# Performance work log

Measured on AMD Instinct MI355X. Metric: run time of the kernel, lower is better.

Reference implementation:

```python
import jax, jax.numpy as jnp
import numpy as np

K = 2            # number of kernel experts (1 common + 1 learned)
TEMPERATURE = 31.0
STRIDE = (2, 2)
KSIZE = 5


def setup_inputs() -> dict:
    key = jax.random.key(0)
    ks = jax.random.split(key, 7)
    B, Cin, H, W = 128, 96, 63, 63
    Cout = 256
    x = jax.random.normal(ks[0], (B, Cin, H, W), jnp.float32)
    common_weight = jax.random.normal(ks[1], (1, Cout, Cin, KSIZE, KSIZE), jnp.float32) * 0.05
    common_bias = jax.random.normal(ks[2], (1, Cout), jnp.float32) * 0.01
    expert_weight = jax.random.normal(ks[3], (1, Cout, Cin, KSIZE, KSIZE), jnp.float32) * 0.05
    expert_bias = jax.random.normal(ks[4], (1, Cout), jnp.float32) * 0.01
    att_w1 = jax.random.normal(ks[5], (24, Cin), jnp.float32) * 0.1   # fc1: 1x1 conv == linear
    att_w2 = jax.random.normal(ks[6], (K, 24), jnp.float32) * 0.1     # fc2
    return {"x": x, "common_weight": common_weight, "common_bias": common_bias,
            "expert_weight": expert_weight, "expert_bias": expert_bias,
            "att_w1": att_w1, "att_w2": att_w2}


def reference(x, common_weight, common_bias, expert_weight, expert_bias, att_w1, att_w2):
    B, Cin, H, W = x.shape
    Cout = common_weight.shape[1]

    # attention2d: global average pool -> fc1 -> relu -> fc2 -> softmax(logits / T)
    pooled = jnp.mean(x, axis=(2, 3))                       # [B, Cin]
    hidden = jax.nn.relu(pooled @ att_w1.T)                 # [B, 24]
    logits = hidden @ att_w2.T                              # [B, K]
    att = jax.nn.softmax(logits / TEMPERATURE, axis=1)      # [B, K]

    # aggregate per-sample kernels: [B,K] @ [K, Cout*Cin*k*k]
    weight = jnp.concatenate([common_weight, expert_weight], axis=0).reshape(K, -1)
    agg_w = (att @ weight).reshape(B * Cout, Cin, KSIZE, KSIZE)
    bias2 = jnp.concatenate([common_bias, expert_bias], axis=0)  # [K, Cout]
    agg_b = (att @ bias2).reshape(-1)                            # [B*Cout]

    # grouped conv with groups = batch_size (per-sample conv)
    xg = x.reshape(1, B * Cin, H, W)
    out = jax.lax.conv_general_dilated(
        xg, agg_w, window_strides=STRIDE, padding='VALID',
        feature_group_count=B,
        dimension_numbers=('NCHW', 'OIHW', 'NCHW'))             # [1, B*Cout, Ho, Wo]
    out = out + agg_b[None, :, None, None]
    Ho, Wo = out.shape[2], out.shape[3]
    return out.reshape(B, Cout, Ho, Wo)
```

## Files before the change

### kernel.cpp

```cpp
#include <hip/hip_runtime.h>
#include <math.h>

#define CIN   96
#define HW_IN 3969
#define WIN   63
#define COUT  256
#define NPIX  900
#define WO    30
#define KTOT  2400
#define NB    128
#define KSTEPS 75
#define AGG_OFF 65536
#define AGG_BYTES ((size_t)NB * 2 * KSTEPS * 8192)

typedef short bf16x8 __attribute__((ext_vector_type(8)));
typedef float f32x4  __attribute__((ext_vector_type(4)));
typedef __attribute__((address_space(1))) const void gas_t;
typedef __attribute__((address_space(3))) void las_t;

__device__ __forceinline__ unsigned pk2(float lo, float hi) {
  unsigned r;
  asm("v_cvt_pk_bf16_f32 %0, %1, %2" : "=v"(r) : "v"(lo), "v"(hi));
  return r;
}

__global__ __launch_bounds__(256) void pool_kernel(const float* __restrict__ x,
                                                   float* __restrict__ pooled) {
  const int ci = blockIdx.x;
  const int b  = blockIdx.y;
  const float* xc = x + ((size_t)b * CIN + ci) * HW_IN;
  const int tid = threadIdx.x, lane = tid & 63, wv = tid >> 6;
  float s = 0.f;
  const int head = (4 - (ci & 3)) & 3;
  if (tid < head) s += xc[tid];
  const float4* x4 = (const float4*)(xc + head);
  const int n4 = (HW_IN - head) >> 2;
  for (int i = tid; i < n4; i += 256) { float4 v = x4[i]; s += (v.x + v.y) + (v.z + v.w); }
  const int done = head + (n4 << 2);
  if (tid < HW_IN - done) s += xc[done + tid];
  #pragma unroll
  for (int off = 32; off > 0; off >>= 1) s += __shfl_xor(s, off, 64);
  __shared__ float part[4];
  if (lane == 0) part[wv] = s;
  __syncthreads();
  if (tid == 0)
    pooled[(size_t)b * CIN + ci] = (part[0] + part[1] + part[2] + part[3]) * (1.0f / HW_IN);
}

__global__ __launch_bounds__(64) void attn_kernel(const float* __restrict__ pooled,
                                                  const float* __restrict__ w1,
                                                  const float* __restrict__ w2,
                                                  float* __restrict__ att) {
  const int b = blockIdx.x;
  const int tid = threadIdx.x;
  __shared__ float hidden[24];
  const float* pb = pooled + (size_t)b * CIN;
  if (tid < 24) {
    float h = 0.f;
    const float* w1r = w1 + tid * CIN;
    for (int ci = 0; ci < CIN; ++ci) h += pb[ci] * w1r[ci];
    hidden[tid] = fmaxf(h, 0.f);
  }
  __syncthreads();
  if (tid == 0) {
    float l0 = 0.f, l1 = 0.f;
    for (int j = 0; j < 24; ++j) { l0 += hidden[j] * w2[j]; l1 += hidden[j] * w2[24 + j]; }
    l0 *= (1.0f / 31.0f); l1 *= (1.0f / 31.0f);
    const float m = fmaxf(l0, l1);
    const float e0 = expf(l0 - m), e1 = expf(l1 - m);
    const float inv = 1.0f / (e0 + e1);
    att[b * 2 + 0] = e0 * inv;
    att[b * 2 + 1] = e1 * inv;
  }
}

__global__ __launch_bounds__(256) void agg_kernel(const float* __restrict__ wc,
                                                  const float* __restrict__ we,
                                                  const float* __restrict__ att,
                                                  unsigned* __restrict__ aggW) {
  const int ks = blockIdx.x;
  const int t  = blockIdx.y;
  const int b  = blockIdx.z;
  const float a0 = att[b * 2 + 0];
  const float a1 = att[b * 2 + 1];
  unsigned* dst = aggW + ((size_t)((b * 2 + t) * KSTEPS + ks) << 11);
  #pragma unroll
  for (int uu = 0; uu < 2; ++uu) {
    const int u = threadIdx.x + uu * 256;
    const int row = u >> 2, slot = u & 3;
    const int oct = slot ^ ((row >> 1) & 3);
    const float* pc = wc + (size_t)(t * 128 + row) * KTOT + ks * 32 + oct * 8;
    const float* pe = we + (size_t)(t * 128 + row) * KTOT + ks * 32 + oct * 8;
    float4 c0 = ((const float4*)pc)[0], c1 = ((const float4*)pc)[1];
    float4 e0 = ((const float4*)pe)[0], e1 = ((const float4*)pe)[1];
    uint4 q;
    q.x = pk2(a0 * c0.x + a1 * e0.x, a0 * c0.y + a1 * e0.y);
    q.y = pk2(a0 * c0.z + a1 * e0.z, a0 * c0.w + a1 * e0.w);
    q.z = pk2(a0 * c1.x + a1 * e1.x, a0 * c1.y + a1 * e1.y);
    q.w = pk2(a0 * c1.z + a1 * e1.z, a0 * c1.w + a1 * e1.w);
    ((uint4*)dst)[u] = q;
  }
}

__global__ __launch_bounds__(256) void conv_pre(
    const float* __restrict__ x,
    const float* __restrict__ bc, const float* __restrict__ be,
    const float* __restrict__ att, const unsigned* __restrict__ aggW,
    float* __restrict__ out) {
  const int flat = (int)(blockIdx.x + (blockIdx.y << 3) + (blockIdx.z << 4));
  const int wg   = ((flat & 7) << 8) | (flat >> 3);
  const int p0 = (wg & 7) * 128;
  const int m0 = ((wg >> 3) & 1) * 128;
  const int b  = wg >> 4;

  __shared__ short As[2][128 * 32];
  __shared__ short Bs[2][128][40];
  __shared__ int   koffAll[KTOT];
  __shared__ float biasS[128];

  const int tid  = threadIdx.x;
  const int wv   = tid >> 6, lane = tid & 63;
  const int quad = lane >> 4, lm = lane & 15;
  const int wm = (wv >> 1) * 64;
  const int wn = (wv & 1) * 64;

  if (tid < 128) {
    const float a0 = att[b * 2 + 0], a1 = att[b * 2 + 1];
    biasS[tid] = a0 * bc[m0 + tid] + a1 * be[m0 + tid];
  }
  for (int k = tid; k < KTOT; k += 256) {
    const int ci = k / 25, r = k - ci * 25;
    const int kh = r / 5,  kw = r - kh * 5;
    koffAll[k] = ci * HW_IN + kh * WIN + kw;
  }

  const int rowT = tid >> 2;
  const int oct  = (tid & 3) * 8;

  const float* xb = x + (size_t)b * (CIN * HW_IN);
  const int pA = p0 + rowT, pB = p0 + rowT + 64;
  const int ohA = pA / WO, owA = pA - ohA * WO;
  const int ohB = pB / WO, owB = pB - ohB * WO;
  const bool vA = pA < NPIX, vB = pB < NPIX;
  const float* xpA = xb + (ohA * 2) * WIN + owA * 2;
  const float* xpB = xb + (ohB * 2) * WIN + owB * 2;

  const char* aggB = (const char*)aggW
                   + ((size_t)((b * 2 + (m0 >> 7)) * KSTEPS) << 13)
                   + (((wv << 7) + lane) << 4);
  const int xoct = quad ^ ((lm >> 1) & 3);

  const f32x4 zero = {0.f, 0.f, 0.f, 0.f};
  f32x4 acc[4][4];
  #pragma unroll
  for (int i = 0; i < 4; ++i)
    #pragma unroll
    for (int j = 0; j < 4; ++j) acc[i][j] = zero;

  __syncthreads();

  {
    __builtin_amdgcn_global_load_lds((gas_t*)aggB, (las_t*)&As[0][wv << 10], 16, 0, 0);
    __builtin_amdgcn_global_load_lds((gas_t*)(aggB + 1024), (las_t*)&As[0][(wv << 10) + 512], 16, 0, 0);
    const int4 ka = *(const int4*)&koffAll[oct];
    const int4 kb = *(const int4*)&koffAll[oct + 4];
    uint4 qa = {0u, 0u, 0u, 0u}, qb = {0u, 0u, 0u, 0u};
    if (vA) {
      qa.x = pk2(xpA[ka.x], xpA[ka.y]); qa.y = pk2(xpA[ka.z], xpA[ka.w]);
      qa.z = pk2(xpA[kb.x], xpA[kb.y]); qa.w = pk2(xpA[kb.z], xpA[kb.w]);
    }
    if (vB) {
      qb.x = pk2(xpB[ka.x], xpB[ka.y]); qb.y = pk2(xpB[ka.z], xpB[ka.w]);
      qb.z = pk2(xpB[kb.x], xpB[kb.y]); qb.w = pk2(xpB[kb.z], xpB[kb.w]);
    }
    *(uint4*)&Bs[0][rowT][oct] = qa;
    *(uint4*)&Bs[0][rowT + 64][oct] = qb;
  }
  __syncthreads();

  int cur = 0;
  for (int ks = 0; ks < KSTEPS - 1; ++ks) {
    const int nxt = cur ^ 1;
    const char* src = aggB + ((size_t)(ks + 1) << 13);
    __builtin_amdgcn_global_load_lds((gas_t*)src, (las_t*)&As[nxt][wv << 10], 16, 0, 0);
    __builtin_amdgcn_global_load_lds((gas_t*)(src + 1024), (las_t*)&As[nxt][(wv << 10) + 512], 16, 0, 0);
    const int k0n = (ks + 1) * 32;
    const int4 ka = *(const int4*)&koffAll[k0n + oct];
    const int4 kb = *(const int4*)&koffAll[k0n + oct + 4];
    float g0 = 0.f, g1 = 0.f, g2 = 0.f, g3 = 0.f, g4 = 0.f, g5 = 0.f, g6 = 0.f, g7 = 0.f;
    float h0 = 0.f, h1 = 0.f, h2 = 0.f, h3 = 0.f, h4 = 0.f, h5 = 0.f, h6 = 0.f, h7 = 0.f;
    if (vA) {
      g0 = xpA[ka.x]; g1 = xpA[ka.y]; g2 = xpA[ka.z]; g3 = xpA[ka.w];
      g4 = xpA[kb.x]; g5 = xpA[kb.y]; g6 = xpA[kb.z]; g7 = xpA[kb.w];
    }
    if (vB) {
      h0 = xpB[ka.x]; h1 = xpB[ka.y]; h2 = xpB[ka.z]; h3 = xpB[ka.w];
      h4 = xpB[kb.x]; h5 = xpB[kb.y]; h6 = xpB[kb.z]; h7 = xpB[kb.w];
    }
    bf16x8 af[4], bfv[4];
    #pragma unroll
    for (int i = 0; i < 4; ++i)
      af[i] = *(const bf16x8*)&As[cur][(wm + i * 16 + lm) * 32 + xoct * 8];
    #pragma unroll
    for (int j = 0; j < 4; ++j)
      bfv[j] = *(const bf16x8*)&Bs[cur][wn + j * 16 + lm][quad * 8];
    #pragma unroll
    for (int i = 0; i < 4; ++i)
      #pragma unroll
      for (int j = 0; j < 4; ++j)
        acc[i][j] = __builtin_amdgcn_mfma_f32_16x16x32_bf16(af[i], bfv[j], acc[i][j], 0, 0, 0);
    uint4 qa, qb;
    qa.x = pk2(g0, g1); qa.y = pk2(g2, g3); qa.z = pk2(g4, g5); qa.w = pk2(g6, g7);
    qb.x = pk2(h0, h1); qb.y = pk2(h2, h3); qb.z = pk2(h4, h5); qb.w = pk2(h6, h7);
    *(uint4*)&Bs[nxt][rowT][oct] = qa;
    *(uint4*)&Bs[nxt][rowT + 64][oct] = qb;
    __syncthreads();
    cur = nxt;
  }

  {
    bf16x8 af[4], bfv[4];
    #pragma unroll
    for (int i = 0; i < 4; ++i)
      af[i] = *(const bf16x8*)&As[cur][(wm + i * 16 + lm) * 32 + xoct * 8];
    #pragma unroll
    for (int j = 0; j < 4; ++j)
      bfv[j] = *(const bf16x8*)&Bs[cur][wn + j * 16 + lm][quad * 8];
    #pragma unroll
    for (int i = 0; i < 4; ++i)
      #pragma unroll
      for (int j = 0; j < 4; ++j)
        acc[i][j] = __builtin_amdgcn_mfma_f32_16x16x32_bf16(af[i], bfv[j], acc[i][j], 0, 0, 0);
  }

  float* outb = out + ((size_t)b * COUT + m0) * NPIX;
  #pragma unroll
  for (int j = 0; j < 4; ++j) {
    const int p = p0 + wn + j * 16 + lm;
    if (p < NPIX) {
      #pragma unroll
      for (int i = 0; i < 4; ++i) {
        #pragma unroll
        for (int r = 0; r < 4; ++r) {
          const int m = wm + i * 16 + quad * 4 + r;
          outb[(size_t)m * NPIX + p] = acc[i][j][r] + biasS[m];
        }
      }
    }
  }
}

__global__ __launch_bounds__(256) void conv_fb(
    const float* __restrict__ x,
    const float* __restrict__ wc, const float* __restrict__ we,
    const float* __restrict__ bc, const float* __restrict__ be,
    const float* __restrict__ att, float* __restrict__ out) {
  const int flat = (int)(blockIdx.x + (blockIdx.y << 3) + (blockIdx.z << 4));
  const int wg   = ((flat & 7) << 8) | (flat >> 3);
  const int p0 = (wg & 7) * 128;
  const int m0 = ((wg >> 3) & 1) * 128;
  const int b  = wg >> 4;

  __shared__ short As[128 * 40];
  __shared__ short Bs[128][40];
  __shared__ int   koffAll[KTOT];
  __shared__ float biasS[128];

  const int tid  = threadIdx.x;
  const int wv   = tid >> 6, lane = tid & 63;
  const int quad = lane >> 4, lm = lane & 15;
  const int wm = (wv >> 1) * 64;
  const int wn = (wv & 1) * 64;

  const float a0 = att[b * 2 + 0];
  const float a1 = att[b * 2 + 1];

  if (tid < 128) biasS[tid] = a0 * bc[m0 + tid] + a1 * be[m0 + tid];
  for (int k = tid; k < KTOT; k += 256) {
    const int ci = k / 25, r = k - ci * 25;
    const int kh = r / 5,  kw = r - kh * 5;
    koffAll[k] = ci * HW_IN + kh * WIN + kw;
  }

  const int rowT = tid >> 2;
  const int oct  = (tid & 3) * 8;

  const float* xb = x + (size_t)b * (CIN * HW_IN);
  const int pA = p0 + rowT, pB = p0 + rowT + 64;
  const int ohA = pA / WO, owA = pA - ohA * WO;
  const int ohB = pB / WO, owB = pB - ohB * WO;
  const bool vA = pA < NPIX, vB = pB < NPIX;
  const float* xpA = xb + (ohA * 2) * WIN + owA * 2;
  const float* xpB = xb + (ohB * 2) * WIN + owB * 2;

  const float* wcr0 = wc + (size_t)(m0 + rowT) * KTOT + oct;
  const float* wer0 = we + (size_t)(m0 + rowT) * KTOT + oct;

  const f32x4 zero = {0.f, 0.f, 0.f, 0.f};
  f32x4 acc[4][4];
  #pragma unroll
  for (int i = 0; i < 4; ++i)
    #pragma unroll
    for (int j = 0; j < 4; ++j) acc[i][j] = zero;

  for (int k0 = 0; k0 < KTOT; k0 += 32) {
    __syncthreads();
    #pragma unroll
    for (int t = 0; t < 2; ++t) {
      const float4* pc = (const float4*)(wcr0 + (size_t)t * 64 * KTOT + k0);
      const float4* pe = (const float4*)(wer0 + (size_t)t * 64 * KTOT + k0);
      float4 c0 = pc[0], c1 = pc[1];
      float4 e0 = pe[0], e1 = pe[1];
      uint4 q;
      q.x = pk2(a0 * c0.x + a1 * e0.x, a0 * c0.y + a1 * e0.y);
      q.y = pk2(a0 * c0.z + a1 * e0.z, a0 * c0.w + a1 * e0.w);
      q.z = pk2(a0 * c1.x + a1 * e1.x, a0 * c1.y + a1 * e1.y);
      q.w = pk2(a0 * c1.z + a1 * e1.z, a0 * c1.w + a1 * e1.w);
      *(uint4*)&As[(rowT + t * 64) * 40 + oct] = q;
    }
    const int4 ka = *(const int4*)&koffAll[k0 + oct];
    const int4 kb = *(const int4*)&koffAll[k0 + oct + 4];
    {
      uint4 q = {0u, 0u, 0u, 0u};
      if (vA) {
        q.x = pk2(xpA[ka.x], xpA[ka.y]); q.y = pk2(xpA[ka.z], xpA[ka.w]);
        q.z = pk2(xpA[kb.x], xpA[kb.y]); q.w = pk2(xpA[kb.z], xpA[kb.w]);
      }
      *(uint4*)&Bs[rowT][oct] = q;
    }
    {
      uint4 q = {0u, 0u, 0u, 0u};
      if (vB) {
        q.x = pk2(xpB[ka.x], xpB[ka.y]); q.y = pk2(xpB[ka.z], xpB[ka.w]);
        q.z = pk2(xpB[kb.x], xpB[kb.y]); q.w = pk2(xpB[kb.z], xpB[kb.w]);
      }
      *(uint4*)&Bs[rowT + 64][oct] = q;
    }
    __syncthreads();
    bf16x8 af[4], bfv[4];
    #pragma unroll
    for (int i = 0; i < 4; ++i) af[i]  = *(const bf16x8*)&As[(wm + i * 16 + lm) * 40 + quad * 8];
    #pragma unroll
    for (int j = 0; j < 4; ++j) bfv[j] = *(const bf16x8*)&Bs[wn + j * 16 + lm][quad * 8];
    #pragma unroll
    for (int i = 0; i < 4; ++i)
      #pragma unroll
      for (int j = 0; j < 4; ++j)
        acc[i][j] = __builtin_amdgcn_mfma_f32_16x16x32_bf16(af[i], bfv[j], acc[i][j], 0, 0, 0);
  }

  float* outb = out + ((size_t)b * COUT + m0) * NPIX;
  #pragma unroll
  for (int j = 0; j < 4; ++j) {
    const int p = p0 + wn + j * 16 + lm;
    if (p < NPIX) {
      #pragma unroll
      for (int i = 0; i < 4; ++i) {
        #pragma unroll
        for (int r = 0; r < 4; ++r) {
          const int m = wm + i * 16 + quad * 4 + r;
          outb[(size_t)m * NPIX + p] = acc[i][j][r] + biasS[m];
        }
      }
    }
  }
}

extern "C" void kernel_launch(void* const* d_in, const int* in_sizes, int n_in,
                              void* d_out, int out_size, void* d_ws, size_t ws_size,
                              hipStream_t stream) {
  (void)in_sizes; (void)n_in; (void)out_size;
  const float* x  = (const float*)d_in[0];
  const float* wc = (const float*)d_in[1];
  const float* bc = (const float*)d_in[2];
  const float* we = (const float*)d_in[3];
  const float* be = (const float*)d_in[4];
  const float* w1 = (const float*)d_in[5];
  const float* w2 = (const float*)d_in[6];
  float* out = (float*)d_out;

  float* att    = (float*)d_ws;
  float* pooled = att + 256;
  unsigned* aggW = (unsigned*)((char*)d_ws + AGG_OFF);

  pool_kernel<<<dim3(CIN, NB), 256, 0, stream>>>(x, pooled);
  attn_kernel<<<NB, 64, 0, stream>>>(pooled, w1, w2, att);

  if (ws_size >= AGG_OFF + AGG_BYTES) {
    agg_kernel<<<dim3(KSTEPS, 2, NB), 256, 0, stream>>>(wc, we, att, aggW);
    conv_pre<<<dim3(8, 2, NB), 256, 0, stream>>>(x, bc, be, att, aggW, out);
  } else {
    conv_fb<<<dim3(8, 2, NB), 256, 0, stream>>>(x, wc, we, bc, be, att, out);
  }
}
```

Before: 745.9 us.

## Deepen conv GEMM pipeline with triple-buffered A and register-prefetched im2col gathers

Restructures the main loop into a deeper software pipeline. Weight tiles are triple-buffered in LDS and prefetched two steps ahead, and the im2col gathers of x are issued two steps ahead into alternating register arrays. Partial waits (vmcnt) plus raw s_barrier replace __syncthreads, MFMA priority is raised with setprio, and the B tile uses an XOR-swizzled unpadded layout. Out-of-range pixels are clamped rather than predicated, which removes branches at the cost of redundant loads, and the extra register arrays raise register pressure.

```diff
diff --git a/kernel.cpp b/kernel.cpp
--- a/kernel.cpp
+++ b/kernel.cpp
@@ -113,8 +113,8 @@
   const int m0 = ((wg >> 3) & 1) * 128;
   const int b  = wg >> 4;
 
-  __shared__ short As[2][128 * 32];
-  __shared__ short Bs[2][128][40];
+  __shared__ short As[3][4096];
+  __shared__ short Bs[2][4096];
   __shared__ int   koffAll[KTOT];
   __shared__ float biasS[128];
 
@@ -136,12 +136,14 @@
 
   const int rowT = tid >> 2;
   const int oct  = (tid & 3) * 8;
+  const int bu   = (tid & 3) ^ ((rowT >> 1) & 3);
 
   const float* xb = x + (size_t)b * (CIN * HW_IN);
   const int pA = p0 + rowT, pB = p0 + rowT + 64;
-  const int ohA = pA / WO, owA = pA - ohA * WO;
-  const int ohB = pB / WO, owB = pB - ohB * WO;
-  const bool vA = pA < NPIX, vB = pB < NPIX;
+  const int pAc = pA < NPIX ? pA : NPIX - 1;
+  const int pBc = pB < NPIX ? pB : NPIX - 1;
+  const int ohA = pAc / WO, owA = pAc - ohA * WO;
+  const int ohB = pBc / WO, owB = pBc - ohB * WO;
   const float* xpA = xb + (ohA * 2) * WIN + owA * 2;
   const float* xpB = xb + (ohB * 2) * WIN + owB * 2;
 
@@ -157,75 +159,95 @@
     #pragma unroll
     for (int j = 0; j < 4; ++j) acc[i][j] = zero;
 
+  float gA[16], gB[16];
+
   __syncthreads();
 
   {
+    const int4 ka = *(const int4*)&koffAll[oct];
+    const int4 kb = *(const int4*)&koffAll[oct + 4];
+    gB[0] = xpA[ka.x]; gB[1] = xpA[ka.y]; gB[2] = xpA[ka.z]; gB[3] = xpA[ka.w];
+    gB[4] = xpA[kb.x]; gB[5] = xpA[kb.y]; gB[6] = xpA[kb.z]; gB[7] = xpA[kb.w];
+    gB[8] = xpB[ka.x]; gB[9] = xpB[ka.y]; gB[10] = xpB[ka.z]; gB[11] = xpB[ka.w];
+    gB[12] = xpB[kb.x]; gB[13] = xpB[kb.y]; gB[14] = xpB[kb.z]; gB[15] = xpB[kb.w];
     __builtin_amdgcn_global_load_lds((gas_t*)aggB, (las_t*)&As[0][wv << 10], 16, 0, 0);
     __builtin_amdgcn_global_load_lds((gas_t*)(aggB + 1024), (las_t*)&As[0][(wv << 10) + 512], 16, 0, 0);
-    const int4 ka = *(const int4*)&koffAll[oct];
-    const int4 kb = *(const int4*)&koffAll[oct + 4];
-    uint4 qa = {0u, 0u, 0u, 0u}, qb = {0u, 0u, 0u, 0u};
-    if (vA) {
-      qa.x = pk2(xpA[ka.x], xpA[ka.y]); qa.y = pk2(xpA[ka.z], xpA[ka.w]);
-      qa.z = pk2(xpA[kb.x], xpA[kb.y]); qa.w = pk2(xpA[kb.z], xpA[kb.w]);
-    }
-    if (vB) {
-      qb.x = pk2(xpB[ka.x], xpB[ka.y]); qb.y = pk2(xpB[ka.z], xpB[ka.w]);
-      qb.z = pk2(xpB[kb.x], xpB[kb.y]); qb.w = pk2(xpB[kb.z], xpB[kb.w]);
-    }
-    *(uint4*)&Bs[0][rowT][oct] = qa;
-    *(uint4*)&Bs[0][rowT + 64][oct] = qb;
+    __builtin_amdgcn_global_load_lds((gas_t*)(aggB + 8192), (las_t*)&As[1][wv << 10], 16, 0, 0);
+    __builtin_amdgcn_global_load_lds((gas_t*)(aggB + 8192 + 1024), (las_t*)&As[1][(wv << 10) + 512], 16, 0, 0);
+    const int4 ka1 = *(const int4*)&koffAll[32 + oct];
+    const int4 kb1 = *(const int4*)&koffAll[32 + oct + 4];
+    gA[0] = xpA[ka1.x]; gA[1] = xpA[ka1.y]; gA[2] = xpA[ka1.z]; gA[3] = xpA[ka1.w];
+    gA[4] = xpA[kb1.x]; gA[5] = xpA[kb1.y]; gA[6] = xpA[kb1.z]; gA[7] = xpA[kb1.w];
+    gA[8] = xpB[ka1.x]; gA[9] = xpB[ka1.y]; gA[10] = xpB[ka1.z]; gA[11] = xpB[ka1.w];
+    gA[12] = xpB[kb1.x]; gA[13] = xpB[kb1.y]; gA[14] = xpB[kb1.z]; gA[15] = xpB[kb1.w];
+    uint4 qa, qb;
+    qa.x = pk2(gB[0], gB[1]);  qa.y = pk2(gB[2], gB[3]);
+    qa.z = pk2(gB[4], gB[5]);  qa.w = pk2(gB[6], gB[7]);
+    qb.x = pk2(gB[8], gB[9]);  qb.y = pk2(gB[10], gB[11]);
+    qb.z = pk2(gB[12], gB[13]); qb.w = pk2(gB[14], gB[15]);
+    *(uint4*)&Bs[0][rowT * 32 + bu * 8] = qa;
+    *(uint4*)&Bs[0][(rowT + 64) * 32 + bu * 8] = qb;
   }
   __syncthreads();
 
-  int cur = 0;
-  for (int ks = 0; ks < KSTEPS - 1; ++ks) {
-    const int nxt = cur ^ 1;
-    const char* src = aggB + ((size_t)(ks + 1) << 13);
-    __builtin_amdgcn_global_load_lds((gas_t*)src, (las_t*)&As[nxt][wv << 10], 16, 0, 0);
-    __builtin_amdgcn_global_load_lds((gas_t*)(src + 1024), (las_t*)&As[nxt][(wv << 10) + 512], 16, 0, 0);
-    const int k0n = (ks + 1) * 32;
-    const int4 ka = *(const int4*)&koffAll[k0n + oct];
-    const int4 kb = *(const int4*)&koffAll[k0n + oct + 4];
-    float g0 = 0.f, g1 = 0.f, g2 = 0.f, g3 = 0.f, g4 = 0.f, g5 = 0.f, g6 = 0.f, g7 = 0.f;
-    float h0 = 0.f, h1 = 0.f, h2 = 0.f, h3 = 0.f, h4 = 0.f, h5 = 0.f, h6 = 0.f, h7 = 0.f;
-    if (vA) {
-      g0 = xpA[ka.x]; g1 = xpA[ka.y]; g2 = xpA[ka.z]; g3 = xpA[ka.w];
-      g4 = xpA[kb.x]; g5 = xpA[kb.y]; g6 = xpA[kb.z]; g7 = xpA[kb.w];
-    }
-    if (vB) {
-      h0 = xpB[ka.x]; h1 = xpB[ka.y]; h2 = xpB[ka.z]; h3 = xpB[ka.w];
-      h4 = xpB[kb.x]; h5 = xpB[kb.y]; h6 = xpB[kb.z]; h7 = xpB[kb.w];
-    }
-    bf16x8 af[4], bfv[4];
-    #pragma unroll
-    for (int i = 0; i < 4; ++i)
-      af[i] = *(const bf16x8*)&As[cur][(wm + i * 16 + lm) * 32 + xoct * 8];
-    #pragma unroll
-    for (int j = 0; j < 4; ++j)
-      bfv[j] = *(const bf16x8*)&Bs[cur][wn + j * 16 + lm][quad * 8];
-    #pragma unroll
-    for (int i = 0; i < 4; ++i)
-      #pragma unroll
-      for (int j = 0; j < 4; ++j)
-        acc[i][j] = __builtin_amdgcn_mfma_f32_16x16x32_bf16(af[i], bfv[j], acc[i][j], 0, 0, 0);
-    uint4 qa, qb;
-    qa.x = pk2(g0, g1); qa.y = pk2(g2, g3); qa.z = pk2(g4, g5); qa.w = pk2(g6, g7);
-    qb.x = pk2(h0, h1); qb.y = pk2(h2, h3); qb.z = pk2(h4, h5); qb.w = pk2(h6, h7);
-    *(uint4*)&Bs[nxt][rowT][oct] = qa;
-    *(uint4*)&Bs[nxt][rowT + 64][oct] = qb;
-    __syncthreads();
-    cur = nxt;
-  }
+  int acur = 0, aw = 2;
+
+  #define CONV_STEP(T, GH, GN, BR, BW)                                            \
+  {                                                                               \
+    const int ksn = ((T) + 2 <= 74) ? (T) + 2 : 74;                               \
+    const int4 ka = *(const int4*)&koffAll[ksn * 32 + oct];                       \
+    const int4 kb = *(const int4*)&koffAll[ksn * 32 + oct + 4];                   \
+    GN[0] = xpA[ka.x]; GN[1] = xpA[ka.y]; GN[2] = xpA[ka.z]; GN[3] = xpA[ka.w];   \
+    GN[4] = xpA[kb.x]; GN[5] = xpA[kb.y]; GN[6] = xpA[kb.z]; GN[7] = xpA[kb.w];   \
+    GN[8] = xpB[ka.x]; GN[9] = xpB[ka.y]; GN[10] = xpB[ka.z]; GN[11] = xpB[ka.w]; \
+    GN[12] = xpB[kb.x]; GN[13] = xpB[kb.y]; GN[14] = xpB[kb.z]; GN[15] = xpB[kb.w]; \
+    const char* srcA = aggB + ((size_t)ksn << 13);                                \
+    __builtin_amdgcn_global_load_lds((gas_t*)srcA, (las_t*)&As[aw][wv << 10], 16, 0, 0); \
+    __builtin_amdgcn_global_load_lds((gas_t*)(srcA + 1024), (las_t*)&As[aw][(wv << 10) + 512], 16, 0, 0); \
+    bf16x8 af[4], bfv[4];                                                         \
+    _Pragma("unroll")                                                             \
+    for (int i = 0; i < 4; ++i)                                                   \
+      af[i] = *(const bf16x8*)&As[acur][(wm + i * 16 + lm) * 32 + xoct * 8];      \
+    _Pragma("unroll")                                                             \
+    for (int j = 0; j < 4; ++j)                                                   \
+      bfv[j] = *(const bf16x8*)&Bs[BR][(wn + j * 16 + lm) * 32 + xoct * 8];       \
+    __builtin_amdgcn_s_setprio(1);                                                \
+    _Pragma("unroll")                                                             \
+    for (int i = 0; i < 4; ++i)                                                   \
+      _Pragma("unroll")                                                           \
+      for (int j = 0; j < 4; ++j)                                                 \
+        acc[i][j] = __builtin_amdgcn_mfma_f32_16x16x32_bf16(af[i], bfv[j], acc[i][j], 0, 0, 0); \
+    __builtin_amdgcn_s_setprio(0);                                                \
+    uint4 qa2, qb2;                                                               \
+    qa2.x = pk2(GH[0], GH[1]);  qa2.y = pk2(GH[2], GH[3]);                        \
+    qa2.z = pk2(GH[4], GH[5]);  qa2.w = pk2(GH[6], GH[7]);                        \
+    qb2.x = pk2(GH[8], GH[9]);  qb2.y = pk2(GH[10], GH[11]);                      \
+    qb2.z = pk2(GH[12], GH[13]); qb2.w = pk2(GH[14], GH[15]);                     \
+    *(uint4*)&Bs[BW][rowT * 32 + bu * 8] = qa2;                                   \
+    *(uint4*)&Bs[BW][(rowT + 64) * 32 + bu * 8] = qb2;                            \
+    __builtin_amdgcn_sched_barrier(0);                                            \
+    asm volatile("s_waitcnt vmcnt(18) lgkmcnt(0)" ::: "memory");                  \
+    __builtin_amdgcn_sched_barrier(0);                                            \
+    __builtin_amdgcn_s_barrier();                                                 \
+    __builtin_amdgcn_sched_barrier(0);                                            \
+    acur = (acur == 2) ? 0 : acur + 1;                                            \
+    aw   = (aw == 2) ? 0 : aw + 1;                                                \
+  }
+
+  for (int t = 0; t < 74; t += 2) {
+    CONV_STEP(t,     gA, gB, 0, 1);
+    CONV_STEP(t + 1, gB, gA, 1, 0);
+  }
+  #undef CONV_STEP
 
   {
     bf16x8 af[4], bfv[4];
     #pragma unroll
     for (int i = 0; i < 4; ++i)
-      af[i] = *(const bf16x8*)&As[cur][(wm + i * 16 + lm) * 32 + xoct * 8];
+      af[i] = *(const bf16x8*)&As[acur][(wm + i * 16 + lm) * 32 + xoct * 8];
     #pragma unroll
     for (int j = 0; j < 4; ++j)
-      bfv[j] = *(const bf16x8*)&Bs[cur][wn + j * 16 + lm][quad * 8];
+      bfv[j] = *(const bf16x8*)&Bs[0][(wn + j * 16 + lm) * 32 + xoct * 8];
     #pragma unroll
     for (int i = 0; i < 4; ++i)
       #pragma unroll
```

Result: slower. 829.3 us (+11.2%).

## Triple-buffer weight tiles with manual vmcnt waits and XOR-swizzle the im2col tile

Applied to the files above, without the earlier changes.

The aggregated-weight tile moves from a double-buffered LDS ring to a triple-buffered one, so the async global-to-LDS load for step ks+2 is issued while step ks computes. The full __syncthreads is replaced by an explicit s_waitcnt vmcnt(2) plus s_barrier, which lets one weight prefetch stay in flight across the barrier. The im2col B tile drops its padded 40-column layout for an unpadded 32-column layout with an XOR swizzle, which cuts LDS bank conflicts and LDS footprint. The risks are subtle ordering bugs in the manual waitcnt and the sched_barrier constraining the compiler's instruction scheduling.

```diff
diff --git a/kernel.cpp b/kernel.cpp
--- a/kernel.cpp
+++ b/kernel.cpp
@@ -113,8 +113,8 @@
   const int m0 = ((wg >> 3) & 1) * 128;
   const int b  = wg >> 4;
 
-  __shared__ short As[2][128 * 32];
-  __shared__ short Bs[2][128][40];
+  __shared__ short As[3][4096];
+  __shared__ short Bs[2][4096];
   __shared__ int   koffAll[KTOT];
   __shared__ float biasS[128];
 
@@ -136,6 +136,7 @@
 
   const int rowT = tid >> 2;
   const int oct  = (tid & 3) * 8;
+  const int bu   = (tid & 3) ^ ((rowT >> 1) & 3);
 
   const float* xb = x + (size_t)b * (CIN * HW_IN);
   const int pA = p0 + rowT, pB = p0 + rowT + 64;
@@ -160,8 +161,6 @@
   __syncthreads();
 
   {
-    __builtin_amdgcn_global_load_lds((gas_t*)aggB, (las_t*)&As[0][wv << 10], 16, 0, 0);
-    __builtin_amdgcn_global_load_lds((gas_t*)(aggB + 1024), (las_t*)&As[0][(wv << 10) + 512], 16, 0, 0);
     const int4 ka = *(const int4*)&koffAll[oct];
     const int4 kb = *(const int4*)&koffAll[oct + 4];
     uint4 qa = {0u, 0u, 0u, 0u}, qb = {0u, 0u, 0u, 0u};
@@ -173,20 +172,22 @@
       qb.x = pk2(xpB[ka.x], xpB[ka.y]); qb.y = pk2(xpB[ka.z], xpB[ka.w]);
       qb.z = pk2(xpB[kb.x], xpB[kb.y]); qb.w = pk2(xpB[kb.z], xpB[kb.w]);
     }
-    *(uint4*)&Bs[0][rowT][oct] = qa;
-    *(uint4*)&Bs[0][rowT + 64][oct] = qb;
+    *(uint4*)&Bs[0][rowT * 32 + bu * 8] = qa;
+    *(uint4*)&Bs[0][(rowT + 64) * 32 + bu * 8] = qb;
+    __builtin_amdgcn_global_load_lds((gas_t*)aggB, (las_t*)&As[0][wv << 10], 16, 0, 0);
+    __builtin_amdgcn_global_load_lds((gas_t*)(aggB + 1024), (las_t*)&As[0][(wv << 10) + 512], 16, 0, 0);
+    __builtin_amdgcn_global_load_lds((gas_t*)(aggB + 8192), (las_t*)&As[1][wv << 10], 16, 0, 0);
+    __builtin_amdgcn_global_load_lds((gas_t*)(aggB + 8192 + 1024), (las_t*)&As[1][(wv << 10) + 512], 16, 0, 0);
   }
   __syncthreads();
 
-  int cur = 0;
+  int acur = 0;
+
   for (int ks = 0; ks < KSTEPS - 1; ++ks) {
-    const int nxt = cur ^ 1;
-    const char* src = aggB + ((size_t)(ks + 1) << 13);
-    __builtin_amdgcn_global_load_lds((gas_t*)src, (las_t*)&As[nxt][wv << 10], 16, 0, 0);
-    __builtin_amdgcn_global_load_lds((gas_t*)(src + 1024), (las_t*)&As[nxt][(wv << 10) + 512], 16, 0, 0);
-    const int k0n = (ks + 1) * 32;
-    const int4 ka = *(const int4*)&koffAll[k0n + oct];
-    const int4 kb = *(const int4*)&koffAll[k0n + oct + 4];
+    const int bcur = ks & 1, bnxt = bcur ^ 1;
+    const int k1 = (ks + 1) << 5;
+    const int4 ka = *(const int4*)&koffAll[k1 + oct];
+    const int4 kb = *(const int4*)&koffAll[k1 + oct + 4];
     float g0 = 0.f, g1 = 0.f, g2 = 0.f, g3 = 0.f, g4 = 0.f, g5 = 0.f, g6 = 0.f, g7 = 0.f;
     float h0 = 0.f, h1 = 0.f, h2 = 0.f, h3 = 0.f, h4 = 0.f, h5 = 0.f, h6 = 0.f, h7 = 0.f;
     if (vA) {
@@ -197,35 +198,44 @@
       h0 = xpB[ka.x]; h1 = xpB[ka.y]; h2 = xpB[ka.z]; h3 = xpB[ka.w];
       h4 = xpB[kb.x]; h5 = xpB[kb.y]; h6 = xpB[kb.z]; h7 = xpB[kb.w];
     }
+    __builtin_amdgcn_sched_barrier(0);
+    {
+      const int ksn = (ks + 2 <= KSTEPS - 1) ? ks + 2 : KSTEPS - 1;
+      const int aw = (acur + 2 >= 3) ? acur - 1 : acur + 2;
+      const char* srcA = aggB + ((size_t)ksn << 13);
+      __builtin_amdgcn_global_load_lds((gas_t*)srcA, (las_t*)&As[aw][wv << 10], 16, 0, 0);
+      __builtin_amdgcn_global_load_lds((gas_t*)(srcA + 1024), (las_t*)&As[aw][(wv << 10) + 512], 16, 0, 0);
+    }
     bf16x8 af[4], bfv[4];
     #pragma unroll
     for (int i = 0; i < 4; ++i)
-      af[i] = *(const bf16x8*)&As[cur][(wm + i * 16 + lm) * 32 + xoct * 8];
+      af[i] = *(const bf16x8*)&As[acur][(wm + i * 16 + lm) * 32 + xoct * 8];
     #pragma unroll
     for (int j = 0; j < 4; ++j)
-      bfv[j] = *(const bf16x8*)&Bs[cur][wn + j * 16 + lm][quad * 8];
+      bfv[j] = *(const bf16x8*)&Bs[bcur][(wn + j * 16 + lm) * 32 + xoct * 8];
     #pragma unroll
     for (int i = 0; i < 4; ++i)
       #pragma unroll
       for (int j = 0; j < 4; ++j)
         acc[i][j] = __builtin_amdgcn_mfma_f32_16x16x32_bf16(af[i], bfv[j], acc[i][j], 0, 0, 0);
-    uint4 qa, qb;
-    qa.x = pk2(g0, g1); qa.y = pk2(g2, g3); qa.z = pk2(g4, g5); qa.w = pk2(g6, g7);
-    qb.x = pk2(h0, h1); qb.y = pk2(h2, h3); qb.z = pk2(h4, h5); qb.w = pk2(h6, h7);
-    *(uint4*)&Bs[nxt][rowT][oct] = qa;
-    *(uint4*)&Bs[nxt][rowT + 64][oct] = qb;
-    __syncthreads();
-    cur = nxt;
+    uint4 qa2, qb2;
+    qa2.x = pk2(g0, g1); qa2.y = pk2(g2, g3); qa2.z = pk2(g4, g5); qa2.w = pk2(g6, g7);
+    qb2.x = pk2(h0, h1); qb2.y = pk2(h2, h3); qb2.z = pk2(h4, h5); qb2.w = pk2(h6, h7);
+    *(uint4*)&Bs[bnxt][rowT * 32 + bu * 8] = qa2;
+    *(uint4*)&Bs[bnxt][(rowT + 64) * 32 + bu * 8] = qb2;
+    asm volatile("s_waitcnt vmcnt(2) lgkmcnt(0)" ::: "memory");
+    __builtin_amdgcn_s_barrier();
+    acur = (acur + 1 == 3) ? 0 : acur + 1;
   }
 
   {
     bf16x8 af[4], bfv[4];
     #pragma unroll
     for (int i = 0; i < 4; ++i)
-      af[i] = *(const bf16x8*)&As[cur][(wm + i * 16 + lm) * 32 + xoct * 8];
+      af[i] = *(const bf16x8*)&As[acur][(wm + i * 16 + lm) * 32 + xoct * 8];
     #pragma unroll
     for (int j = 0; j < 4; ++j)
-      bfv[j] = *(const bf16x8*)&Bs[cur][wn + j * 16 + lm][quad * 8];
+      bfv[j] = *(const bf16x8*)&Bs[(KSTEPS - 1) & 1][(wn + j * 16 + lm) * 32 + xoct * 8];
     #pragma unroll
     for (int i = 0; i < 4; ++i)
       #pragma unroll
```

Measured after the change: 758.7 us. Within noise of the previous version (+1.7%).

## Merge both Cout halves into one 512-thread block to share im2col gather

Applied to the files above, without the earlier changes.

Each block now covers all 256 output channels for a 128-pixel tile, using 8 waves, where previously two blocks each handled 128 channels. The im2col gather of x, with its scattered global loads and bf16 conversion, is therefore done once per pixel tile instead of twice, and each thread now gathers one row instead of two. The aggregated weight buffer is interleaved per k-step so the block loads a contiguous 16 KB A tile. The B tile drops its padded stride in favour of an XOR swizzle. LDS use per block grows and the grid halves, which may reduce occupancy and latency hiding.

```diff
diff --git a/kernel.cpp b/kernel.cpp
--- a/kernel.cpp
+++ b/kernel.cpp
@@ -11,7 +11,7 @@
 #define NB    128
 #define KSTEPS 75
 #define AGG_OFF 65536
-#define AGG_BYTES ((size_t)NB * 2 * KSTEPS * 8192)
+#define AGG_BYTES ((size_t)NB * KSTEPS * 16384)
 
 typedef short bf16x8 __attribute__((ext_vector_type(8)));
 typedef float f32x4  __attribute__((ext_vector_type(4)));
@@ -83,7 +83,7 @@
   const int b  = blockIdx.z;
   const float a0 = att[b * 2 + 0];
   const float a1 = att[b * 2 + 1];
-  unsigned* dst = aggW + ((size_t)((b * 2 + t) * KSTEPS + ks) << 11);
+  unsigned* dst = aggW + (((size_t)b * KSTEPS + ks) << 12) + (t << 11);
   #pragma unroll
   for (int uu = 0; uu < 2; ++uu) {
     const int u = threadIdx.x + uu * 256;
@@ -102,21 +102,20 @@
   }
 }
 
-__global__ __launch_bounds__(256) void conv_pre(
+__global__ __launch_bounds__(512) void conv_pre(
     const float* __restrict__ x,
     const float* __restrict__ bc, const float* __restrict__ be,
     const float* __restrict__ att, const unsigned* __restrict__ aggW,
     float* __restrict__ out) {
-  const int flat = (int)(blockIdx.x + (blockIdx.y << 3) + (blockIdx.z << 4));
-  const int wg   = ((flat & 7) << 8) | (flat >> 3);
+  const int flat = (int)(blockIdx.x + (blockIdx.z << 3));
+  const int wg   = ((flat & 7) << 7) | (flat >> 3);
   const int p0 = (wg & 7) * 128;
-  const int m0 = ((wg >> 3) & 1) * 128;
-  const int b  = wg >> 4;
-
-  __shared__ short As[2][128 * 32];
-  __shared__ short Bs[2][128][40];
+  const int b  = wg >> 3;
+
+  __shared__ short As[2][256 * 32];
+  __shared__ short Bs[2][128 * 32];
   __shared__ int   koffAll[KTOT];
-  __shared__ float biasS[128];
+  __shared__ float biasS[COUT];
 
   const int tid  = threadIdx.x;
   const int wv   = tid >> 6, lane = tid & 63;
@@ -124,11 +123,11 @@
   const int wm = (wv >> 1) * 64;
   const int wn = (wv & 1) * 64;
 
-  if (tid < 128) {
+  if (tid < COUT) {
     const float a0 = att[b * 2 + 0], a1 = att[b * 2 + 1];
-    biasS[tid] = a0 * bc[m0 + tid] + a1 * be[m0 + tid];
-  }
-  for (int k = tid; k < KTOT; k += 256) {
+    biasS[tid] = a0 * bc[tid] + a1 * be[tid];
+  }
+  for (int k = tid; k < KTOT; k += 512) {
     const int ci = k / 25, r = k - ci * 25;
     const int kh = r / 5,  kw = r - kh * 5;
     koffAll[k] = ci * HW_IN + kh * WIN + kw;
@@ -136,17 +135,16 @@
 
   const int rowT = tid >> 2;
   const int oct  = (tid & 3) * 8;
+  const int bu   = (tid & 3) ^ ((rowT >> 1) & 3);
 
   const float* xb = x + (size_t)b * (CIN * HW_IN);
-  const int pA = p0 + rowT, pB = p0 + rowT + 64;
+  const int pA = p0 + rowT;
   const int ohA = pA / WO, owA = pA - ohA * WO;
-  const int ohB = pB / WO, owB = pB - ohB * WO;
-  const bool vA = pA < NPIX, vB = pB < NPIX;
+  const bool vA = pA < NPIX;
   const float* xpA = xb + (ohA * 2) * WIN + owA * 2;
-  const float* xpB = xb + (ohB * 2) * WIN + owB * 2;
 
   const char* aggB = (const char*)aggW
-                   + ((size_t)((b * 2 + (m0 >> 7)) * KSTEPS) << 13)
+                   + ((size_t)b * KSTEPS << 14)
                    + (((wv << 7) + lane) << 4);
   const int xoct = quad ^ ((lm >> 1) & 3);
 
@@ -164,68 +162,55 @@
     __builtin_amdgcn_global_load_lds((gas_t*)(aggB + 1024), (las_t*)&As[0][(wv << 10) + 512], 16, 0, 0);
     const int4 ka = *(const int4*)&koffAll[oct];
     const int4 kb = *(const int4*)&koffAll[oct + 4];
-    uint4 qa = {0u, 0u, 0u, 0u}, qb = {0u, 0u, 0u, 0u};
+    uint4 qa = {0u, 0u, 0u, 0u};
     if (vA) {
       qa.x = pk2(xpA[ka.x], xpA[ka.y]); qa.y = pk2(xpA[ka.z], xpA[ka.w]);
       qa.z = pk2(xpA[kb.x], xpA[kb.y]); qa.w = pk2(xpA[kb.z], xpA[kb.w]);
     }
-    if (vB) {
-      qb.x = pk2(xpB[ka.x], xpB[ka.y]); qb.y = pk2(xpB[ka.z], xpB[ka.w]);
-      qb.z = pk2(xpB[kb.x], xpB[kb.y]); qb.w = pk2(xpB[kb.z], xpB[kb.w]);
-    }
-    *(uint4*)&Bs[0][rowT][oct] = qa;
-    *(uint4*)&Bs[0][rowT + 64][oct] = qb;
+    *(uint4*)&Bs[0][rowT * 32 + bu * 8] = qa;
   }
   __syncthreads();
 
-  int cur = 0;
   for (int ks = 0; ks < KSTEPS - 1; ++ks) {
-    const int nxt = cur ^ 1;
-    const char* src = aggB + ((size_t)(ks + 1) << 13);
+    const int cur = ks & 1, nxt = cur ^ 1;
+    const char* src = aggB + ((size_t)(ks + 1) << 14);
     __builtin_amdgcn_global_load_lds((gas_t*)src, (las_t*)&As[nxt][wv << 10], 16, 0, 0);
     __builtin_amdgcn_global_load_lds((gas_t*)(src + 1024), (las_t*)&As[nxt][(wv << 10) + 512], 16, 0, 0);
-    const int k0n = (ks + 1) * 32;
-    const int4 ka = *(const int4*)&koffAll[k0n + oct];
-    const int4 kb = *(const int4*)&koffAll[k0n + oct + 4];
+    const int k1 = (ks + 1) << 5;
+    const int4 ka = *(const int4*)&koffAll[k1 + oct];
+    const int4 kb = *(const int4*)&koffAll[k1 + oct + 4];
     float g0 = 0.f, g1 = 0.f, g2 = 0.f, g3 = 0.f, g4 = 0.f, g5 = 0.f, g6 = 0.f, g7 = 0.f;
-    float h0 = 0.f, h1 = 0.f, h2 = 0.f, h3 = 0.f, h4 = 0.f, h5 = 0.f, h6 = 0.f, h7 = 0.f;
     if (vA) {
       g0 = xpA[ka.x]; g1 = xpA[ka.y]; g2 = xpA[ka.z]; g3 = xpA[ka.w];
       g4 = xpA[kb.x]; g5 = xpA[kb.y]; g6 = xpA[kb.z]; g7 = xpA[kb.w];
     }
-    if (vB) {
-      h0 = xpB[ka.x]; h1 = xpB[ka.y]; h2 = xpB[ka.z]; h3 = xpB[ka.w];
-      h4 = xpB[kb.x]; h5 = xpB[kb.y]; h6 = xpB[kb.z]; h7 = xpB[kb.w];
-    }
     bf16x8 af[4], bfv[4];
     #pragma unroll
     for (int i = 0; i < 4; ++i)
       af[i] = *(const bf16x8*)&As[cur][(wm + i * 16 + lm) * 32 + xoct * 8];
     #pragma unroll
     for (int j = 0; j < 4; ++j)
-      bfv[j] = *(const bf16x8*)&Bs[cur][wn + j * 16 + lm][quad * 8];
+      bfv[j] = *(const bf16x8*)&Bs[cur][(wn + j * 16 + lm) * 32 + xoct * 8];
     #pragma unroll
     for (int i = 0; i < 4; ++i)
       #pragma unroll
       for (int j = 0; j < 4; ++j)
         acc[i][j] = __builtin_amdgcn_mfma_f32_16x16x32_bf16(af[i], bfv[j], acc[i][j], 0, 0, 0);
-    uint4 qa, qb;
+    uint4 qa;
     qa.x = pk2(g0, g1); qa.y = pk2(g2, g3); qa.z = pk2(g4, g5); qa.w = pk2(g6, g7);
-    qb.x = pk2(h0, h1); qb.y = pk2(h2, h3); qb.z = pk2(h4, h5); qb.w = pk2(h6, h7);
-    *(uint4*)&Bs[nxt][rowT][oct] = qa;
-    *(uint4*)&Bs[nxt][rowT + 64][oct] = qb;
+    *(uint4*)&Bs[nxt][rowT * 32 + bu * 8] = qa;
     __syncthreads();
-    cur = nxt;
   }
 
   {
+    const int cur = (KSTEPS - 1) & 1;
     bf16x8 af[4], bfv[4];
     #pragma unroll
     for (int i = 0; i < 4; ++i)
       af[i] = *(const bf16x8*)&As[cur][(wm + i * 16 + lm) * 32 + xoct * 8];
     #pragma unroll
     for (int j = 0; j < 4; ++j)
-      bfv[j] = *(const bf16x8*)&Bs[cur][wn + j * 16 + lm][quad * 8];
+      bfv[j] = *(const bf16x8*)&Bs[cur][(wn + j * 16 + lm) * 32 + xoct * 8];
     #pragma unroll
     for (int i = 0; i < 4; ++i)
       #pragma unroll
@@ -233,7 +218,7 @@
         acc[i][j] = __builtin_amdgcn_mfma_f32_16x16x32_bf16(af[i], bfv[j], acc[i][j], 0, 0, 0);
   }
 
-  float* outb = out + ((size_t)b * COUT + m0) * NPIX;
+  float* outb = out + (size_t)b * COUT * NPIX;
   #pragma unroll
   for (int j = 0; j < 4; ++j) {
     const int p = p0 + wn + j * 16 + lm;
@@ -388,7 +373,7 @@
 
   if (ws_size >= AGG_OFF + AGG_BYTES) {
     agg_kernel<<<dim3(KSTEPS, 2, NB), 256, 0, stream>>>(wc, we, att, aggW);
-    conv_pre<<<dim3(8, 2, NB), 256, 0, stream>>>(x, bc, be, att, aggW, out);
+    conv_pre<<<dim3(8, 1, NB), 512, 0, stream>>>(x, bc, be, att, aggW, out);
   } else {
     conv_fb<<<dim3(8, 2, NB), 256, 0, stream>>>(x, wc, we, bc, be, att, out);
   }
```

Result: faster. 598.6 us (-19.7%).
